# Performance work log

Measured on AMD Instinct MI355X. Metric: run time of the kernel, lower is better.

Reference implementation:

```python
import jax, jax.numpy as jnp
import numpy as np

B, NIN, H1, H2, NOUT, COND, FC = 64, 512, 1024, 1024, 512, 64, 1


def _made_masks():
    rng = np.random.RandomState(0)
    d_in = np.arange(1, NIN + 1)
    d1 = rng.randint(1, NIN, size=H1)
    d2 = rng.randint(1, NIN, size=H2)
    d_out = np.arange(1, NOUT + 1)
    m0 = (d1[:, None] >= d_in[None, :]).astype(np.float32)   # (H1, NIN)
    m1 = (d2[:, None] >= d1[None, :]).astype(np.float32)     # (H2, H1)
    m2 = (d_out[:, None] > d2[None, :]).astype(np.float32)   # (NOUT, H2)
    return m0, m1, m2


def setup_inputs() -> dict:
    key = jax.random.key(0)
    ks = jax.random.split(key, 20)
    m0, m1, m2 = _made_masks()

    def lin(k, o, i):  # fan-in scaled weight
        return jax.random.normal(k, (o, i), jnp.float32) / np.float32(np.sqrt(i))

    def vec(k, n):
        return jax.random.normal(k, (n,), jnp.float32) * 0.01

    return {
        "x": jax.random.normal(ks[0], (B, NIN), jnp.float32),
        "u": jax.random.normal(ks[1], (B, COND), jnp.float32),
        "mask0": jnp.asarray(m0), "mask1": jnp.asarray(m1), "mask2": jnp.asarray(m2),
        "W0": lin(ks[2], H1, NIN), "W1": lin(ks[3], H2, H1), "W2": lin(ks[4], NOUT, H2),
        "a0_w": lin(ks[5], FC * NIN, COND), "a0_b": vec(ks[6], FC * NIN),
        "b0_w": lin(ks[7], FC * H1, COND), "b0_b": vec(ks[8], FC * H1),
        "a1_w": lin(ks[9], FC * H1, COND), "a1_b": vec(ks[10], FC * H1),
        "b1_w": lin(ks[11], FC * H2, COND), "b1_b": vec(ks[12], FC * H2),
        "a2_w": lin(ks[13], FC * H2, COND), "a2_b": vec(ks[14], FC * H2),
        "b2_w": lin(ks[15], FC * NOUT, COND), "b2_b": vec(ks[16], FC * NOUT),
    }


def _cml(x, u, W, m, aw, ab, bw, bb):
    # ConditionedMaskedLinear.forward
    Bb = x.shape[0]
    o, i = W.shape
    f1 = (u @ aw.T + ab).reshape(Bb, FC, i)      # (B, F, in)
    f2 = (u @ bw.T + bb).reshape(Bb, o, FC)      # (B, out, F)
    cond_mask = jax.nn.sigmoid(jnp.einsum('bfi,bof->boi', f1, f2)) * (m * W)
    return jnp.einsum('boi,bi->bo', cond_mask, x)


def reference(x, u, mask0, mask1, mask2, W0, W1, W2,
              a0_w, a0_b, b0_w, b0_b,
              a1_w, a1_b, b1_w, b1_b,
              a2_w, a2_b, b2_w, b2_b):
    # ConditionalStrNN.forward applies ONLY the ConditionedMaskedLinear layers
    # (activations/norms in net_list are skipped by the isinstance check).
    h = _cml(x, u, W0, mask0, a0_w, a0_b, b0_w, b0_b)
    h = _cml(h, u, W1, mask1, a1_w, a1_b, b1_w, b1_b)
    h = _cml(h, u, W2, mask2, a2_w, a2_b, b2_w, b2_b)
    return h
```

## Files before the change

kernel.cpp:

```cpp
#include <hip/hip_runtime.h>

#define BB    64
#define NIN   512
#define H1D   1024
#define H2D   1024
#define NOUTD 512
#define CONDD 64
#define L2E   1.4426950408889634f

__global__ __launch_bounds__(256) void prep_kernel(
    const float* __restrict__ x,  const float* __restrict__ u,
    const float* __restrict__ a0w, const float* __restrict__ a0b,
    const float* __restrict__ b0w, const float* __restrict__ b0b,
    const float* __restrict__ a1w, const float* __restrict__ a1b,
    const float* __restrict__ b1w, const float* __restrict__ b1b,
    const float* __restrict__ a2w, const float* __restrict__ a2b,
    const float* __restrict__ b2w, const float* __restrict__ b2b,
    float* __restrict__ AX0, float* __restrict__ AX1, float* __restrict__ AX2,
    float* __restrict__ C0t, float* __restrict__ C1t, float* __restrict__ C2t)
{
    __shared__ float lds[64 * 65];
    const int tid = threadIdx.x;
    const int bid = blockIdx.x;

    if (bid < 320) {
        for (int e = tid; e < BB * CONDD; e += 256)
            lds[(e & 63) * 65 + (e >> 6)] = u[e];
        __syncthreads();

        const int b   = tid & 63;
        const int wid = __builtin_amdgcn_readfirstlane(tid >> 6);
        const int r0  = bid * 16 + wid * 4;

        const float* w; const float* bias; float* out; int stride; float scale; int lr0;
        if      (r0 <  512) { w = a0w; bias = a0b; out = AX0; stride = 2; scale = L2E; lr0 = r0;        }
        else if (r0 < 1536) { w = b0w; bias = b0b; out = C0t; stride = 1; scale = 1.f; lr0 = r0 -  512; }
        else if (r0 < 2560) { w = a1w; bias = a1b; out = AX1; stride = 2; scale = L2E; lr0 = r0 - 1536; }
        else if (r0 < 3584) { w = b1w; bias = b1b; out = C1t; stride = 1; scale = 1.f; lr0 = r0 - 2560; }
        else if (r0 < 4608) { w = a2w; bias = a2b; out = AX2; stride = 2; scale = L2E; lr0 = r0 - 3584; }
        else                { w = b2w; bias = b2b; out = C2t; stride = 1; scale = 1.f; lr0 = r0 - 4608; }

        const float* __restrict__ w0 = w + (lr0 + 0) * CONDD;
        const float* __restrict__ w1 = w + (lr0 + 1) * CONDD;
        const float* __restrict__ w2 = w + (lr0 + 2) * CONDD;
        const float* __restrict__ w3 = w + (lr0 + 3) * CONDD;
        float acc0 = bias[lr0 + 0], acc1 = bias[lr0 + 1];
        float acc2 = bias[lr0 + 2], acc3 = bias[lr0 + 3];
        #pragma unroll
        for (int k = 0; k < CONDD; ++k) {
            const float uv = lds[k * 65 + b];
            acc0 = fmaf(w0[k], uv, acc0);
            acc1 = fmaf(w1[k], uv, acc1);
            acc2 = fmaf(w2[k], uv, acc2);
            acc3 = fmaf(w3[k], uv, acc3);
        }
        out[((lr0 + 0) * 64 + b) * stride] = acc0 * scale;
        out[((lr0 + 1) * 64 + b) * stride] = acc1 * scale;
        out[((lr0 + 2) * 64 + b) * stride] = acc2 * scale;
        out[((lr0 + 3) * 64 + b) * stride] = acc3 * scale;
    } else {
        const int i0 = (bid - 320) * 64;
        for (int e = tid; e < 64 * 64; e += 256) {
            int r = e >> 6, c = e & 63;
            lds[c * 65 + r] = x[r * NIN + i0 + c];
        }
        __syncthreads();
        for (int e = tid; e < 64 * 64; e += 256) {
            int r = e >> 6, c = e & 63;
            AX0[((i0 + r) * 64 + c) * 2 + 1] = lds[r * 65 + c];
        }
    }
}

template<int I, int OT, bool FINAL>
__device__ __forceinline__ void gated_body(
    const float2* __restrict__ AX, const float* __restrict__ Ct,
    const float*  __restrict__ M,  const float* __restrict__ W,
    float* __restrict__ out)
{
    constexpr int NW  = 16;
    constexpr int ICW = I / NW;
    __shared__ float4 mw4[(OT * I) / 4];
    __shared__ float  red[NW][OT][64];

    const int tid = threadIdx.x;
    const int b   = tid & 63;
    const int wid = __builtin_amdgcn_readfirstlane(tid >> 6);
    const int o0  = blockIdx.x * OT;

    {
        const float4* __restrict__ Mp = (const float4*)(M + (size_t)o0 * I);
        const float4* __restrict__ Wp = (const float4*)(W + (size_t)o0 * I);
        for (int e = tid; e < (OT * I) / 4; e += NW * 64) {
            const float4 a = Mp[e];
            const float4 c = Wp[e];
            float4 r;
            r.x = a.x * c.x; r.y = a.y * c.y; r.z = a.z * c.z; r.w = a.w * c.w;
            mw4[e] = r;
        }
    }

    float cc[OT], acc[OT];
    #pragma unroll
    for (int oo = 0; oo < OT; ++oo) {
        cc[oo]  = Ct[(o0 + oo) * 64 + b];
        acc[oo] = 0.f;
    }
    __syncthreads();

    const int ibase = wid * ICW;
    const float*  __restrict__ mwp = ((const float*)mw4) + ibase;
    const float2* __restrict__ axp = AX + (size_t)ibase * 64 + b;

    #pragma unroll 8
    for (int ii = 0; ii < ICW; ++ii) {
        const float2 ax = axp[(size_t)ii * 64];
        #pragma unroll
        for (int oo = 0; oo < OT; ++oo) {
            const float mw = mwp[oo * I + ii];
            const float t  = __builtin_amdgcn_exp2f(-(ax.x * cc[oo]));
            const float s  = __builtin_amdgcn_rcpf(1.f + t);
            acc[oo] = fmaf(s, mw * ax.y, acc[oo]);
        }
    }

    #pragma unroll
    for (int oo = 0; oo < OT; ++oo) red[wid][oo][b] = acc[oo];
    __syncthreads();
    if (tid < OT * 64) {
        const int oo = tid >> 6, bb = tid & 63;
        float v = 0.f;
        #pragma unroll
        for (int w16 = 0; w16 < NW; ++w16) v += red[w16][oo][bb];
        if (FINAL) out[bb * NOUTD + (o0 + oo)] = v;
        else       out[((o0 + oo) * 64 + bb) * 2 + 1] = v;
    }
}

__global__ __launch_bounds__(1024) void gated_l1(
    const float2* __restrict__ AX, const float* __restrict__ Ct,
    const float* __restrict__ M, const float* __restrict__ W, float* __restrict__ out)
{ gated_body<NIN, 4, false>(AX, Ct, M, W, out); }

__global__ __launch_bounds__(1024) void gated_l2(
    const float2* __restrict__ AX, const float* __restrict__ Ct,
    const float* __restrict__ M, const float* __restrict__ W, float* __restrict__ out)
{ gated_body<H1D, 4, false>(AX, Ct, M, W, out); }

__global__ __launch_bounds__(1024) void gated_l3(
    const float2* __restrict__ AX, const float* __restrict__ Ct,
    const float* __restrict__ M, const float* __restrict__ W, float* __restrict__ out)
{ gated_body<H2D, 2, true>(AX, Ct, M, W, out); }

extern "C" void kernel_launch(void* const* d_in, const int* in_sizes, int n_in,
                              void* d_out, int out_size, void* d_ws, size_t ws_size,
                              hipStream_t stream) {
    (void)in_sizes; (void)n_in; (void)out_size; (void)ws_size;
    const float* x   = (const float*)d_in[0];
    const float* u   = (const float*)d_in[1];
    const float* m0  = (const float*)d_in[2];
    const float* m1  = (const float*)d_in[3];
    const float* m2  = (const float*)d_in[4];
    const float* W0  = (const float*)d_in[5];
    const float* W1  = (const float*)d_in[6];
    const float* W2  = (const float*)d_in[7];
    const float* a0w = (const float*)d_in[8];  const float* a0b = (const float*)d_in[9];
    const float* b0w = (const float*)d_in[10]; const float* b0b = (const float*)d_in[11];
    const float* a1w = (const float*)d_in[12]; const float* a1b = (const float*)d_in[13];
    const float* b1w = (const float*)d_in[14]; const float* b1b = (const float*)d_in[15];
    const float* a2w = (const float*)d_in[16]; const float* a2b = (const float*)d_in[17];
    const float* b2w = (const float*)d_in[18]; const float* b2b = (const float*)d_in[19];

    float* ws  = (float*)d_ws;
    float* AX0 = ws;
    float* AX1 = ws + 65536;
    float* AX2 = ws + 196608;
    float* C0t = ws + 327680;
    float* C1t = ws + 393216;
    float* C2t = ws + 458752;
    float* out = (float*)d_out;

    prep_kernel<<<328, 256, 0, stream>>>(x, u,
        a0w, a0b, b0w, b0b, a1w, a1b, b1w, b1b, a2w, a2b, b2w, b2b,
        AX0, AX1, AX2, C0t, C1t, C2t);

    gated_l1<<<H1D / 4,   1024, 0, stream>>>((const float2*)AX0, C0t, m0, W0, AX1);
    gated_l2<<<H2D / 4,   1024, 0, stream>>>((const float2*)AX1, C1t, m1, W1, AX2);
    gated_l3<<<NOUTD / 2, 1024, 0, stream>>>((const float2*)AX2, C2t, m2, W2, out);
}
```

Before: 144.4 us.

## Fuse prep and three gated layers into one persistent kernel with grid barriers

Merges the prep kernel and the three gated-layer kernels into a single 256-block kernel, using atomic-counter grid barriers between stages in place of separate kernel launches. The prep work is repacked into fewer, larger blocks of 1024 threads. This removes launch gaps and inter-kernel drain, but depends on all 256 blocks being resident at once because it uses a normal launch rather than a cooperative one, and it adds a memset plus spin-wait cost.

Measured after the change: 216.6 us. +50.0%, slower.

```diff
diff --git a/kernel.cpp b/kernel.cpp
--- a/kernel.cpp
+++ b/kernel.cpp
@@ -8,7 +8,90 @@
 #define CONDD 64
 #define L2E   1.4426950408889634f
 
-__global__ __launch_bounds__(256) void prep_kernel(
+__device__ __forceinline__ void grid_barrier(unsigned* __restrict__ bar, int phase)
+{
+    __syncthreads();
+    if (threadIdx.x == 0) {
+        __threadfence();
+        __hip_atomic_fetch_add(&bar[phase], 1u, __ATOMIC_ACQ_REL,
+                               __HIP_MEMORY_SCOPE_AGENT);
+        while (__hip_atomic_load(&bar[phase], __ATOMIC_ACQUIRE,
+                                 __HIP_MEMORY_SCOPE_AGENT) < 256u) {
+            __builtin_amdgcn_s_sleep(8);
+        }
+        __threadfence();
+    }
+    __syncthreads();
+}
+
+template<int I, int OT, bool FINAL>
+__device__ __forceinline__ void gated_body(
+    float* __restrict__ lds,
+    const float2* __restrict__ AX, const float* __restrict__ Ct,
+    const float*  __restrict__ M,  const float* __restrict__ W,
+    float* __restrict__ out, int bid)
+{
+    constexpr int NW  = 16;
+    constexpr int ICW = I / NW;
+
+    const int tid = threadIdx.x;
+    const int b   = tid & 63;
+    const int wid = __builtin_amdgcn_readfirstlane(tid >> 6);
+    const int o0  = bid * OT;
+
+    float4* __restrict__ mw4 = (float4*)lds;
+    float*  __restrict__ red = lds + OT * I;
+
+    {
+        const float4* __restrict__ Mp = (const float4*)(M + (size_t)o0 * I);
+        const float4* __restrict__ Wp = (const float4*)(W + (size_t)o0 * I);
+        for (int e = tid; e < (OT * I) / 4; e += NW * 64) {
+            const float4 a = Mp[e];
+            const float4 c = Wp[e];
+            float4 r;
+            r.x = a.x * c.x; r.y = a.y * c.y; r.z = a.z * c.z; r.w = a.w * c.w;
+            mw4[e] = r;
+        }
+    }
+
+    float cc[OT], acc[OT];
+    #pragma unroll
+    for (int oo = 0; oo < OT; ++oo) {
+        cc[oo]  = Ct[(o0 + oo) * 64 + b];
+        acc[oo] = 0.f;
+    }
+    __syncthreads();
+
+    const int ibase = wid * ICW;
+    const float*  __restrict__ mwp = lds + ibase;
+    const float2* __restrict__ axp = AX + (size_t)ibase * 64 + b;
+
+    #pragma unroll 8
+    for (int ii = 0; ii < ICW; ++ii) {
+        const float2 ax = axp[(size_t)ii * 64];
+        #pragma unroll
+        for (int oo = 0; oo < OT; ++oo) {
+            const float mw = mwp[oo * I + ii];
+            const float t  = __builtin_amdgcn_exp2f(-(ax.x * cc[oo]));
+            const float s  = __builtin_amdgcn_rcpf(1.f + t);
+            acc[oo] = fmaf(s, mw * ax.y, acc[oo]);
+        }
+    }
+
+    #pragma unroll
+    for (int oo = 0; oo < OT; ++oo) red[(wid * OT + oo) * 64 + b] = acc[oo];
+    __syncthreads();
+    if (tid < OT * 64) {
+        const int oo = tid >> 6, bb = tid & 63;
+        float v = 0.f;
+        #pragma unroll
+        for (int w16 = 0; w16 < NW; ++w16) v += red[(w16 * OT + oo) * 64 + bb];
+        if (FINAL) out[bb * NOUTD + (o0 + oo)] = v;
+        else       out[((o0 + oo) * 64 + bb) * 2 + 1] = v;
+    }
+}
+
+__global__ __launch_bounds__(1024) void fused_kernel(
     const float* __restrict__ x,  const float* __restrict__ u,
     const float* __restrict__ a0w, const float* __restrict__ a0b,
     const float* __restrict__ b0w, const float* __restrict__ b0b,
@@ -16,29 +99,33 @@
     const float* __restrict__ b1w, const float* __restrict__ b1b,
     const float* __restrict__ a2w, const float* __restrict__ a2b,
     const float* __restrict__ b2w, const float* __restrict__ b2b,
+    const float* __restrict__ m0, const float* __restrict__ W0,
+    const float* __restrict__ m1, const float* __restrict__ W1,
+    const float* __restrict__ m2, const float* __restrict__ W2,
     float* __restrict__ AX0, float* __restrict__ AX1, float* __restrict__ AX2,
-    float* __restrict__ C0t, float* __restrict__ C1t, float* __restrict__ C2t)
+    float* __restrict__ C0t, float* __restrict__ C1t, float* __restrict__ C2t,
+    unsigned* __restrict__ bar, float* __restrict__ out)
 {
-    __shared__ float lds[64 * 65];
+    __shared__ float lds[8192];
     const int tid = threadIdx.x;
     const int bid = blockIdx.x;
 
-    if (bid < 320) {
-        for (int e = tid; e < BB * CONDD; e += 256)
+    if (bid < 80) {
+        for (int e = tid; e < BB * CONDD; e += 1024)
             lds[(e & 63) * 65 + (e >> 6)] = u[e];
         __syncthreads();
 
         const int b   = tid & 63;
         const int wid = __builtin_amdgcn_readfirstlane(tid >> 6);
-        const int r0  = bid * 16 + wid * 4;
-
-        const float* w; const float* bias; float* out; int stride; float scale; int lr0;
-        if      (r0 <  512) { w = a0w; bias = a0b; out = AX0; stride = 2; scale = L2E; lr0 = r0;        }
-        else if (r0 < 1536) { w = b0w; bias = b0b; out = C0t; stride = 1; scale = 1.f; lr0 = r0 -  512; }
-        else if (r0 < 2560) { w = a1w; bias = a1b; out = AX1; stride = 2; scale = L2E; lr0 = r0 - 1536; }
-        else if (r0 < 3584) { w = b1w; bias = b1b; out = C1t; stride = 1; scale = 1.f; lr0 = r0 - 2560; }
-        else if (r0 < 4608) { w = a2w; bias = a2b; out = AX2; stride = 2; scale = L2E; lr0 = r0 - 3584; }
-        else                { w = b2w; bias = b2b; out = C2t; stride = 1; scale = 1.f; lr0 = r0 - 4608; }
+        const int r0  = bid * 64 + wid * 4;
+
+        const float* w; const float* bias; float* o; int stride; float scale; int lr0;
+        if      (r0 <  512) { w = a0w; bias = a0b; o = AX0; stride = 2; scale = L2E; lr0 = r0;        }
+        else if (r0 < 1536) { w = b0w; bias = b0b; o = C0t; stride = 1; scale = 1.f; lr0 = r0 -  512; }
+        else if (r0 < 2560) { w = a1w; bias = a1b; o = AX1; stride = 2; scale = L2E; lr0 = r0 - 1536; }
+        else if (r0 < 3584) { w = b1w; bias = b1b; o = C1t; stride = 1; scale = 1.f; lr0 = r0 - 2560; }
+        else if (r0 < 4608) { w = a2w; bias = a2b; o = AX2; stride = 2; scale = L2E; lr0 = r0 - 3584; }
+        else                { w = b2w; bias = b2b; o = C2t; stride = 1; scale = 1.f; lr0 = r0 - 4608; }
 
         const float* __restrict__ w0 = w + (lr0 + 0) * CONDD;
         const float* __restrict__ w1 = w + (lr0 + 1) * CONDD;
@@ -54,103 +141,30 @@
             acc2 = fmaf(w2[k], uv, acc2);
             acc3 = fmaf(w3[k], uv, acc3);
         }
-        out[((lr0 + 0) * 64 + b) * stride] = acc0 * scale;
-        out[((lr0 + 1) * 64 + b) * stride] = acc1 * scale;
-        out[((lr0 + 2) * 64 + b) * stride] = acc2 * scale;
-        out[((lr0 + 3) * 64 + b) * stride] = acc3 * scale;
-    } else {
-        const int i0 = (bid - 320) * 64;
-        for (int e = tid; e < 64 * 64; e += 256) {
+        o[((lr0 + 0) * 64 + b) * stride] = acc0 * scale;
+        o[((lr0 + 1) * 64 + b) * stride] = acc1 * scale;
+        o[((lr0 + 2) * 64 + b) * stride] = acc2 * scale;
+        o[((lr0 + 3) * 64 + b) * stride] = acc3 * scale;
+    } else if (bid < 88) {
+        const int i0 = (bid - 80) * 64;
+        for (int e = tid; e < 64 * 64; e += 1024) {
             int r = e >> 6, c = e & 63;
             lds[c * 65 + r] = x[r * NIN + i0 + c];
         }
         __syncthreads();
-        for (int e = tid; e < 64 * 64; e += 256) {
+        for (int e = tid; e < 64 * 64; e += 1024) {
             int r = e >> 6, c = e & 63;
             AX0[((i0 + r) * 64 + c) * 2 + 1] = lds[r * 65 + c];
         }
     }
-}
-
-template<int I, int OT, bool FINAL>
-__device__ __forceinline__ void gated_body(
-    const float2* __restrict__ AX, const float* __restrict__ Ct,
-    const float*  __restrict__ M,  const float* __restrict__ W,
-    float* __restrict__ out)
-{
-    constexpr int NW  = 16;
-    constexpr int ICW = I / NW;
-    __shared__ float4 mw4[(OT * I) / 4];
-    __shared__ float  red[NW][OT][64];
-
-    const int tid = threadIdx.x;
-    const int b   = tid & 63;
-    const int wid = __builtin_amdgcn_readfirstlane(tid >> 6);
-    const int o0  = blockIdx.x * OT;
-
-    {
-        const float4* __restrict__ Mp = (const float4*)(M + (size_t)o0 * I);
-        const float4* __restrict__ Wp = (const float4*)(W + (size_t)o0 * I);
-        for (int e = tid; e < (OT * I) / 4; e += NW * 64) {
-            const float4 a = Mp[e];
-            const float4 c = Wp[e];
-            float4 r;
-            r.x = a.x * c.x; r.y = a.y * c.y; r.z = a.z * c.z; r.w = a.w * c.w;
-            mw4[e] = r;
-        }
-    }
-
-    float cc[OT], acc[OT];
-    #pragma unroll
-    for (int oo = 0; oo < OT; ++oo) {
-        cc[oo]  = Ct[(o0 + oo) * 64 + b];
-        acc[oo] = 0.f;
-    }
-    __syncthreads();
-
-    const int ibase = wid * ICW;
-    const float*  __restrict__ mwp = ((const float*)mw4) + ibase;
-    const float2* __restrict__ axp = AX + (size_t)ibase * 64 + b;
-
-    #pragma unroll 8
-    for (int ii = 0; ii < ICW; ++ii) {
-        const float2 ax = axp[(size_t)ii * 64];
-        #pragma unroll
-        for (int oo = 0; oo < OT; ++oo) {
-            const float mw = mwp[oo * I + ii];
-            const float t  = __builtin_amdgcn_exp2f(-(ax.x * cc[oo]));
-            const float s  = __builtin_amdgcn_rcpf(1.f + t);
-            acc[oo] = fmaf(s, mw * ax.y, acc[oo]);
-        }
-    }
-
-    #pragma unroll
-    for (int oo = 0; oo < OT; ++oo) red[wid][oo][b] = acc[oo];
-    __syncthreads();
-    if (tid < OT * 64) {
-        const int oo = tid >> 6, bb = tid & 63;
-        float v = 0.f;
-        #pragma unroll
-        for (int w16 = 0; w16 < NW; ++w16) v += red[w16][oo][bb];
-        if (FINAL) out[bb * NOUTD + (o0 + oo)] = v;
-        else       out[((o0 + oo) * 64 + bb) * 2 + 1] = v;
-    }
-}
-
-__global__ __launch_bounds__(1024) void gated_l1(
-    const float2* __restrict__ AX, const float* __restrict__ Ct,
-    const float* __restrict__ M, const float* __restrict__ W, float* __restrict__ out)
-{ gated_body<NIN, 4, false>(AX, Ct, M, W, out); }
-
-__global__ __launch_bounds__(1024) void gated_l2(
-    const float2* __restrict__ AX, const float* __restrict__ Ct,
-    const float* __restrict__ M, const float* __restrict__ W, float* __restrict__ out)
-{ gated_body<H1D, 4, false>(AX, Ct, M, W, out); }
-
-__global__ __launch_bounds__(1024) void gated_l3(
-    const float2* __restrict__ AX, const float* __restrict__ Ct,
-    const float* __restrict__ M, const float* __restrict__ W, float* __restrict__ out)
-{ gated_body<H2D, 2, true>(AX, Ct, M, W, out); }
+
+    grid_barrier(bar, 0);
+    gated_body<NIN, 4, false>(lds, (const float2*)AX0, C0t, m0, W0, AX1, bid);
+    grid_barrier(bar, 1);
+    gated_body<H1D, 4, false>(lds, (const float2*)AX1, C1t, m1, W1, AX2, bid);
+    grid_barrier(bar, 2);
+    gated_body<H2D, 2, true>(lds, (const float2*)AX2, C2t, m2, W2, out, bid);
+}
 
 extern "C" void kernel_launch(void* const* d_in, const int* in_sizes, int n_in,
                               void* d_out, int out_size, void* d_ws, size_t ws_size,
@@ -178,13 +192,24 @@
     float* C0t = ws + 327680;
     float* C1t = ws + 393216;
     float* C2t = ws + 458752;
+    unsigned* bar = (unsigned*)(ws + 524288);
     float* out = (float*)d_out;
 
-    prep_kernel<<<328, 256, 0, stream>>>(x, u,
+    hipMemsetAsync((void*)bar, 0, 64, stream);
+
+    void* args[] = {
+        (void*)&x, (void*)&u,
+        (void*)&a0w, (void*)&a0b, (void*)&b0w, (void*)&b0b,
+        (void*)&a1w, (void*)&a1b, (void*)&b1w, (void*)&b1b,
+        (void*)&a2w, (void*)&a2b, (void*)&b2w, (void*)&b2b,
+        (void*)&m0, (void*)&W0, (void*)&m1, (void*)&W1, (void*)&m2, (void*)&W2,
+        (void*)&AX0, (void*)&AX1, (void*)&AX2,
+        (void*)&C0t, (void*)&C1t, (void*)&C2t,
+        (void*)&bar, (void*)&out
+    };
+    (void)args;
+    fused_kernel<<<256, 1024, 0, stream>>>(x, u,
         a0w, a0b, b0w, b0b, a1w, a1b, b1w, b1b, a2w, a2b, b2w, b2b,
-        AX0, AX1, AX2, C0t, C1t, C2t);
-
-    gated_l1<<<H1D / 4,   1024, 0, stream>>>((const float2*)AX0, C0t, m0, W0, AX1);
-    gated_l2<<<H2D / 4,   1024, 0, stream>>>((const float2*)AX1, C1t, m1, W1, AX2);
-    gated_l3<<<NOUTD / 2, 1024, 0, stream>>>((const float2*)AX2, C2t, m2, W2, out);
-}
+        m0, W0, m1, W1, m2, W2,
+        AX0, AX1, AX2, C0t, C1t, C2t, bar, out);
+}
```
